# Kernel optimization log

Hardware: AMD Instinct MI355X
Metric: run time of the kernel (lower is better)

The kernel has to match this reference:

```python
import jax, jax.numpy as jnp
import numpy as np

N_NODES = 50000


def _gcn_norm(edge_index, num_nodes):
    # PyG gcn_norm with add_self_loops=True, edge_weight=1
    loops = jnp.arange(num_nodes, dtype=edge_index.dtype)
    src = jnp.concatenate([edge_index[0], loops])
    dst = jnp.concatenate([edge_index[1], loops])
    deg = jax.ops.segment_sum(jnp.ones_like(dst, dtype=jnp.float32), dst,
                              num_segments=num_nodes)
    deg_inv_sqrt = jnp.where(deg > 0, jax.lax.rsqrt(jnp.maximum(deg, 1.0)), 0.0)
    norm = deg_inv_sqrt[src] * deg_inv_sqrt[dst]  # [E + N]
    return src, dst, norm


def _gcn_conv(x, src, dst, norm, W, b, num_nodes):
    h = x @ W                                 # [N, out] dense transform first
    msg = h[src] * norm[:, None]              # gather + scale, [E+N, out]
    out = jax.ops.segment_sum(msg, dst, num_segments=num_nodes)  # scatter-add
    return out + b


def setup_inputs() -> dict:
    key = jax.random.key(0)
    k1, k2, k3, k4, k5 = jax.random.split(key, 5)
    in_ch, out_ch = 128, 64
    hid = 2 * out_ch
    x = jax.random.normal(k1, (N_NODES, in_ch), dtype=jnp.float32)
    edge_index = jax.random.randint(k2, (2, 800000), 0, N_NODES, dtype=jnp.int64)
    # Glorot init like PyG GCNConv
    W1 = jax.random.normal(k3, (in_ch, hid), dtype=jnp.float32) * (1.0 / np.sqrt(in_ch))
    b1 = jnp.zeros((hid,), dtype=jnp.float32)
    W2 = jax.random.normal(k4, (hid, out_ch), dtype=jnp.float32) * (1.0 / np.sqrt(hid))
    b2 = jnp.zeros((out_ch,), dtype=jnp.float32)
    return {"x": x, "edge_index": edge_index, "W1": W1, "b1": b1,
            "W2": W2, "b2": b2}


def reference(x, edge_index, W1, b1, W2, b2):
    num_nodes = x.shape[0]
    src, dst, norm = _gcn_norm(edge_index, num_nodes)
    h = _gcn_conv(x, src, dst, norm, W1, b1, num_nodes)
    h = jax.nn.relu(h)
    return _gcn_conv(h, src, dst, norm, W2, b2, num_nodes)
```

## Files before the change

kernel.cpp:

```cpp
#include <hip/hip_runtime.h>

#define N_NODES 50000
#define N_EDGES 800000
#define IN_CH   128
#define HID     128
#define OUT_CH  64

#define NBUCK 196
#define BUCKW 256
#define XPAD  136

typedef __attribute__((ext_vector_type(8))) short bf16x8;
typedef __attribute__((ext_vector_type(4))) float f32x4;
typedef unsigned short ushort_t;

__device__ __forceinline__ unsigned short f2bf(float f) {
    unsigned u = __float_as_uint(f);
    u += 0x7fffu + ((u >> 16) & 1u);
    return (unsigned short)(u >> 16);
}
__device__ __forceinline__ unsigned pack2(float a, float b) {
    return (unsigned)f2bf(a) | ((unsigned)f2bf(b) << 16);
}
__device__ __forceinline__ float bf_lo(unsigned u) { return __uint_as_float(u << 16); }
__device__ __forceinline__ float bf_hi(unsigned u) { return __uint_as_float(u & 0xffff0000u); }


__global__ void k_zero_small(int* __restrict__ bcnt) {
    if (threadIdx.x < NBUCK) bcnt[threadIdx.x] = 0;
}

__global__ __launch_bounds__(256) void kb_hist(const int* __restrict__ dst,
                                               int* __restrict__ bcnt) {
    __shared__ int lh[NBUCK];
    for (int i = threadIdx.x; i < NBUCK; i += 256) lh[i] = 0;
    __syncthreads();
    int base = blockIdx.x * 8192;
#pragma unroll 4
    for (int k = 0; k < 32; ++k) {
        int e = base + k * 256 + threadIdx.x;
        if (e < N_EDGES) atomicAdd(&lh[dst[e] >> 8], 1);
    }
    __syncthreads();
    for (int i = threadIdx.x; i < NBUCK; i += 256)
        if (lh[i]) atomicAdd(&bcnt[i], lh[i]);
}

__global__ __launch_bounds__(256) void kb_scan(const int* __restrict__ bcnt,
                                               int* __restrict__ bbase,
                                               int* __restrict__ bcur,
                                               int* __restrict__ row_ptr) {
    __shared__ int s[256];
    int t = threadIdx.x;
    int v = (t < NBUCK) ? bcnt[t] : 0;
    s[t] = v;
    __syncthreads();
    for (int off = 1; off < 256; off <<= 1) {
        int u = (t >= off) ? s[t - off] : 0;
        __syncthreads();
        s[t] += u;
        __syncthreads();
    }
    int excl = s[t] - v;
    if (t < NBUCK) { bbase[t] = excl; bcur[t] = excl; }
    if (t == 0) { bbase[NBUCK] = N_EDGES; row_ptr[N_NODES] = N_EDGES; }
}

__global__ __launch_bounds__(256) void kb_scatter(const int* __restrict__ src,
                                                  const int* __restrict__ dst,
                                                  int* __restrict__ bcur,
                                                  uint2* __restrict__ rec) {
    __shared__ int lh[NBUCK];
    __shared__ int gbase[NBUCK];
    for (int i = threadIdx.x; i < NBUCK; i += 256) lh[i] = 0;
    __syncthreads();
    int base = blockIdx.x * 4096;
#pragma unroll 4
    for (int k = 0; k < 16; ++k) {
        int e = base + k * 256 + threadIdx.x;
        if (e < N_EDGES) atomicAdd(&lh[dst[e] >> 8], 1);
    }
    __syncthreads();
    for (int i = threadIdx.x; i < NBUCK; i += 256) {
        int c = lh[i];
        gbase[i] = c ? atomicAdd(&bcur[i], c) : 0;
    }
    __syncthreads();
    for (int i = threadIdx.x; i < NBUCK; i += 256) lh[i] = 0;
    __syncthreads();
#pragma unroll 4
    for (int k = 0; k < 16; ++k) {
        int e = base + k * 256 + threadIdx.x;
        if (e < N_EDGES) {
            int d = dst[e], b = d >> 8;
            int rk = atomicAdd(&lh[b], 1);
            rec[gbase[b] + rk] = make_uint2((unsigned)src[e], (unsigned)d);
        }
    }
}

__global__ __launch_bounds__(256) void kc_csr(const int* __restrict__ bbase,
                                              const uint2* __restrict__ rec,
                                              int* __restrict__ row_ptr,
                                              float* __restrict__ dis,
                                              int* __restrict__ col) {
    __shared__ int lh[BUCKW];
    __shared__ int cur[BUCKW];
    __shared__ int s[BUCKW];
    const int b = blockIdx.x, t = threadIdx.x;
    const int lo = bbase[b], hi = bbase[b + 1];
    lh[t] = 0;
    __syncthreads();
    for (int j = lo + t; j < hi; j += 256)
        atomicAdd(&lh[(int)rec[j].y - (b << 8)], 1);
    __syncthreads();
    int deg = lh[t];
    s[t] = deg;
    __syncthreads();
    for (int off = 1; off < 256; off <<= 1) {
        int u = (t >= off) ? s[t - off] : 0;
        __syncthreads();
        s[t] += u;
        __syncthreads();
    }
    int gp = lo + s[t] - deg;
    int node = (b << 8) + t;
    if (node < N_NODES) {
        row_ptr[node] = gp;
        dis[node] = rsqrtf((float)deg + 1.0f);
    }
    cur[t] = gp;
    __syncthreads();
    for (int j = lo + t; j < hi; j += 256) {
        uint2 r = rec[j];
        int pos = atomicAdd(&cur[(int)r.y - (b << 8)], 1);
        col[pos] = (int)r.x;
    }
}


__global__ __launch_bounds__(256) void k_prep(const float* __restrict__ W1,
                                              const float* __restrict__ W2,
                                              ushort_t* __restrict__ W1t,
                                              ushort_t* __restrict__ W2t) {
    int i = blockIdx.x * 256 + threadIdx.x;
    if (i < 128 * 128) {
        int k = i >> 7, c = i & 127;
        W1t[c * 128 + k] = f2bf(W1[k * 128 + c]);
    } else {
        int j = i - 128 * 128;
        if (j < 128 * 64) {
            int k = j >> 6, c = j & 63;
            W2t[c * 128 + k] = f2bf(W2[k * 64 + c]);
        }
    }
}


__global__ __launch_bounds__(256) void k_gemm1(const float* __restrict__ x,
                                               const ushort_t* __restrict__ W1t,
                                               const float* __restrict__ dis,
                                               ushort_t* __restrict__ g) {
    __shared__ ushort_t xs[64 * XPAD];
    __shared__ ushort_t ws[128 * XPAD];
    const int tid = threadIdx.x;
    const int row0 = blockIdx.x * 64;

    for (int i = tid; i < 64 * 32; i += 256) {
        int r = i >> 5, k4 = (i & 31) << 2;
        int gr = row0 + r;
        float4 v = make_float4(0.f, 0.f, 0.f, 0.f);
        if (gr < N_NODES) v = *(const float4*)&x[(long)gr * IN_CH + k4];
        ushort4 u;
        u.x = f2bf(v.x); u.y = f2bf(v.y); u.z = f2bf(v.z); u.w = f2bf(v.w);
        *(ushort4*)&xs[r * XPAD + k4] = u;
    }
    for (int i = tid; i < 128 * 16; i += 256) {
        int c = i >> 4, seg = i & 15;
        *(uint4*)&ws[c * XPAD + seg * 8] = *(const uint4*)&W1t[c * 128 + seg * 8];
    }
    __syncthreads();

    const int w = tid >> 6, lane = tid & 63;
    const int m = lane & 15, q = lane >> 4;
    const ushort_t* arow = &xs[(w * 16 + m) * XPAD + q * 8];
    const ushort_t* brow = &ws[m * XPAD + q * 8];

    f32x4 acc[8] = {};
#pragma unroll
    for (int k0 = 0; k0 < 128; k0 += 32) {
        bf16x8 a = *(const bf16x8*)(arow + k0);
#pragma unroll
        for (int nt = 0; nt < 8; ++nt) {
            bf16x8 b = *(const bf16x8*)(brow + nt * 16 * XPAD + k0);
            acc[nt] = __builtin_amdgcn_mfma_f32_16x16x32_bf16(a, b, acc[nt], 0, 0, 0);
        }
    }

#pragma unroll
    for (int reg = 0; reg < 4; ++reg) {
        int gr = row0 + w * 16 + q * 4 + reg;
        if (gr < N_NODES) {
            float d = dis[gr];
#pragma unroll
            for (int nt = 0; nt < 8; ++nt)
                g[(long)gr * HID + nt * 16 + m] = f2bf(acc[nt][reg] * d);
        }
    }
}


__global__ __launch_bounds__(256) void k_gemm2(const ushort_t* __restrict__ a1,
                                               const ushort_t* __restrict__ W2t,
                                               const float* __restrict__ dis,
                                               ushort_t* __restrict__ g) {
    __shared__ ushort_t xs[64 * XPAD];
    __shared__ ushort_t ws[64 * XPAD];
    const int tid = threadIdx.x;
    const int row0 = blockIdx.x * 64;

    for (int i = tid; i < 64 * 16; i += 256) {
        int r = i >> 4, seg = i & 15;
        int gr = row0 + r;
        uint4 v = make_uint4(0u, 0u, 0u, 0u);
        if (gr < N_NODES) v = *(const uint4*)&a1[(long)gr * HID + seg * 8];
        *(uint4*)&xs[r * XPAD + seg * 8] = v;
    }
    for (int i = tid; i < 64 * 16; i += 256) {
        int c = i >> 4, seg = i & 15;
        *(uint4*)&ws[c * XPAD + seg * 8] = *(const uint4*)&W2t[c * 128 + seg * 8];
    }
    __syncthreads();

    const int w = tid >> 6, lane = tid & 63;
    const int m = lane & 15, q = lane >> 4;
    const ushort_t* arow = &xs[(w * 16 + m) * XPAD + q * 8];
    const ushort_t* brow = &ws[m * XPAD + q * 8];

    f32x4 acc[4] = {};
#pragma unroll
    for (int k0 = 0; k0 < 128; k0 += 32) {
        bf16x8 a = *(const bf16x8*)(arow + k0);
#pragma unroll
        for (int nt = 0; nt < 4; ++nt) {
            bf16x8 b = *(const bf16x8*)(brow + nt * 16 * XPAD + k0);
            acc[nt] = __builtin_amdgcn_mfma_f32_16x16x32_bf16(a, b, acc[nt], 0, 0, 0);
        }
    }

#pragma unroll
    for (int reg = 0; reg < 4; ++reg) {
        int gr = row0 + w * 16 + q * 4 + reg;
        if (gr < N_NODES) {
            float d = dis[gr];
#pragma unroll
            for (int nt = 0; nt < 4; ++nt)
                g[(long)gr * OUT_CH + nt * 16 + m] = f2bf(acc[nt][reg] * d);
        }
    }
}


__global__ __launch_bounds__(256) void k_agg1(const int* __restrict__ row_ptr,
                                              const int* __restrict__ col,
                                              const float* __restrict__ dis,
                                              const ushort_t* __restrict__ g1,
                                              const float* __restrict__ b1,
                                              ushort_t* __restrict__ a1) {
    int r = blockIdx.x * 4 + (threadIdx.x >> 6);
    if (r >= N_NODES) return;
    const int lane = threadIdx.x & 63;
    const int q = lane >> 4;
    const int seg = lane & 15;
    const int cl = seg << 3;
    const uint4* G = (const uint4*)g1;
    const int beg = row_ptr[r], end = row_ptr[r + 1];

    float acc[8] = {};
    int e = beg + q;
    for (; e + 4 < end; e += 8) {
        int s0 = col[e], s1 = col[e + 4];
        uint4 u0 = G[(long)s0 * 16 + seg];
        uint4 u1 = G[(long)s1 * 16 + seg];
        acc[0] += bf_lo(u0.x); acc[1] += bf_hi(u0.x);
        acc[2] += bf_lo(u0.y); acc[3] += bf_hi(u0.y);
        acc[4] += bf_lo(u0.z); acc[5] += bf_hi(u0.z);
        acc[6] += bf_lo(u0.w); acc[7] += bf_hi(u0.w);
        acc[0] += bf_lo(u1.x); acc[1] += bf_hi(u1.x);
        acc[2] += bf_lo(u1.y); acc[3] += bf_hi(u1.y);
        acc[4] += bf_lo(u1.z); acc[5] += bf_hi(u1.z);
        acc[6] += bf_lo(u1.w); acc[7] += bf_hi(u1.w);
    }
    if (e < end) {
        int s = col[e];
        uint4 u = G[(long)s * 16 + seg];
        acc[0] += bf_lo(u.x); acc[1] += bf_hi(u.x);
        acc[2] += bf_lo(u.y); acc[3] += bf_hi(u.y);
        acc[4] += bf_lo(u.z); acc[5] += bf_hi(u.z);
        acc[6] += bf_lo(u.w); acc[7] += bf_hi(u.w);
    }
#pragma unroll
    for (int off = 16; off < 64; off <<= 1)
#pragma unroll
        for (int j = 0; j < 8; ++j) acc[j] += __shfl_xor(acc[j], off);

    if (q == 0) {
        uint4 u = G[(long)r * 16 + seg];
        acc[0] += bf_lo(u.x); acc[1] += bf_hi(u.x);
        acc[2] += bf_lo(u.y); acc[3] += bf_hi(u.y);
        acc[4] += bf_lo(u.z); acc[5] += bf_hi(u.z);
        acc[6] += bf_lo(u.w); acc[7] += bf_hi(u.w);
        const float d = dis[r];
        float o[8];
#pragma unroll
        for (int j = 0; j < 8; ++j) o[j] = fmaxf(acc[j] * d + b1[cl + j], 0.f);
        uint4 pw;
        pw.x = pack2(o[0], o[1]); pw.y = pack2(o[2], o[3]);
        pw.z = pack2(o[4], o[5]); pw.w = pack2(o[6], o[7]);
        *(uint4*)&a1[(long)r * HID + cl] = pw;
    }
}


__global__ __launch_bounds__(256) void k_agg2(const int* __restrict__ row_ptr,
                                              const int* __restrict__ col,
                                              const float* __restrict__ dis,
                                              const ushort_t* __restrict__ g3,
                                              const float* __restrict__ b2,
                                              float* __restrict__ out) {
    int r = blockIdx.x * 4 + (threadIdx.x >> 6);
    if (r >= N_NODES) return;
    const int lane = threadIdx.x & 63;
    const int q = lane >> 3;
    const int seg = lane & 7;
    const int cl = seg << 3;
    const uint4* G = (const uint4*)g3;
    const int beg = row_ptr[r], end = row_ptr[r + 1];

    float acc[8] = {};
    int e = beg + q;
    for (; e + 8 < end; e += 16) {
        int s0 = col[e], s1 = col[e + 8];
        uint4 u0 = G[(long)s0 * 8 + seg];
        uint4 u1 = G[(long)s1 * 8 + seg];
        acc[0] += bf_lo(u0.x); acc[1] += bf_hi(u0.x);
        acc[2] += bf_lo(u0.y); acc[3] += bf_hi(u0.y);
        acc[4] += bf_lo(u0.z); acc[5] += bf_hi(u0.z);
        acc[6] += bf_lo(u0.w); acc[7] += bf_hi(u0.w);
        acc[0] += bf_lo(u1.x); acc[1] += bf_hi(u1.x);
        acc[2] += bf_lo(u1.y); acc[3] += bf_hi(u1.y);
        acc[4] += bf_lo(u1.z); acc[5] += bf_hi(u1.z);
        acc[6] += bf_lo(u1.w); acc[7] += bf_hi(u1.w);
    }
    if (e < end) {
        int s = col[e];
        uint4 u = G[(long)s * 8 + seg];
        acc[0] += bf_lo(u.x); acc[1] += bf_hi(u.x);
        acc[2] += bf_lo(u.y); acc[3] += bf_hi(u.y);
        acc[4] += bf_lo(u.z); acc[5] += bf_hi(u.z);
        acc[6] += bf_lo(u.w); acc[7] += bf_hi(u.w);
    }
#pragma unroll
    for (int off = 8; off < 64; off <<= 1)
#pragma unroll
        for (int j = 0; j < 8; ++j) acc[j] += __shfl_xor(acc[j], off);

    if (q == 0) {
        uint4 u = G[(long)r * 8 + seg];
        acc[0] += bf_lo(u.x); acc[1] += bf_hi(u.x);
        acc[2] += bf_lo(u.y); acc[3] += bf_hi(u.y);
        acc[4] += bf_lo(u.z); acc[5] += bf_hi(u.z);
        acc[6] += bf_lo(u.w); acc[7] += bf_hi(u.w);
        const float d = dis[r];
        float4 o0, o1;
        o0.x = acc[0] * d + b2[cl + 0];
        o0.y = acc[1] * d + b2[cl + 1];
        o0.z = acc[2] * d + b2[cl + 2];
        o0.w = acc[3] * d + b2[cl + 3];
        o1.x = acc[4] * d + b2[cl + 4];
        o1.y = acc[5] * d + b2[cl + 5];
        o1.z = acc[6] * d + b2[cl + 6];
        o1.w = acc[7] * d + b2[cl + 7];
        *(float4*)&out[(long)r * OUT_CH + cl] = o0;
        *(float4*)&out[(long)r * OUT_CH + cl + 4] = o1;
    }
}


extern "C" void kernel_launch(void* const* d_in, const int* in_sizes, int n_in,
                              void* d_out, int out_size, void* d_ws, size_t ws_size,
                              hipStream_t stream) {
    const float* x   = (const float*)d_in[0];
    const int*   ei  = (const int*)d_in[1];
    const float* W1  = (const float*)d_in[2];
    const float* b1  = (const float*)d_in[3];
    const float* W2  = (const float*)d_in[4];
    const float* b2  = (const float*)d_in[5];
    float* out = (float*)d_out;

    const int* src = ei;
    const int* dst = ei + N_EDGES;

    char* p = (char*)d_ws;
    uint2* rec   = (uint2*)p;             p += (long)N_EDGES * 8;
    int* col     = (int*)p;               p += (long)N_EDGES * 4;
    int* row_ptr = (int*)p;               p += 50064 * 4;
    int* bcnt    = (int*)p;               p += 256 * 4;
    int* bbase   = (int*)p;               p += 256 * 4;
    int* bcur    = (int*)p;               p += 256 * 4;
    float* dis   = (float*)p;             p += 50048 * 4;
    ushort_t* W1t = (ushort_t*)p;         p += 128 * 128 * 2;
    ushort_t* W2t = (ushort_t*)p;         p += 128 * 64 * 2;
    ushort_t* g1  = (ushort_t*)p;         p += (long)N_NODES * HID * 2;
    ushort_t* a1  = (ushort_t*)p;         p += (long)N_NODES * HID * 2;
    ushort_t* g3  = (ushort_t*)p;

    const int B = 256;

    k_zero_small<<<1, B, 0, stream>>>(bcnt);
    k_prep<<<96, B, 0, stream>>>(W1, W2, W1t, W2t);
    kb_hist<<<(N_EDGES + 8191) / 8192, B, 0, stream>>>(dst, bcnt);
    kb_scan<<<1, B, 0, stream>>>(bcnt, bbase, bcur, row_ptr);
    kb_scatter<<<(N_EDGES + 4095) / 4096, B, 0, stream>>>(src, dst, bcur, rec);
    kc_csr<<<NBUCK, B, 0, stream>>>(bbase, rec, row_ptr, dis, col);

    k_gemm1<<<(N_NODES + 63) / 64, B, 0, stream>>>(x, W1t, dis, g1);
    k_agg1<<<(N_NODES + 3) / 4, B, 0, stream>>>(row_ptr, col, dis, g1, b1, a1);
    k_gemm2<<<(N_NODES + 63) / 64, B, 0, stream>>>(a1, W2t, dis, g3);
    k_agg2<<<(N_NODES + 3) / 4, B, 0, stream>>>(row_ptr, col, dis, g3, b2, out);
}
```

Measured before the change: 208.2 us.

## Fuse layer-1 aggregation into second GEMM and fold bucket scan into consumers

Layer-1 aggregation (gather, bias, ReLU) now feeds LDS directly in a new aggregate-then-MFMA kernel, so the a1 intermediate is never written to or read back from global memory. The bucket prefix scan is recomputed inside the scatter and CSR kernels, and the zeroing kernel is merged with weight prep. Together these drop several launches. The edge records are packed into 32 bits (16-bit source plus low 8 bits of destination), halving the record traffic. The trade-off is parallelism: each wave now aggregates 16 rows one after another instead of one row per wave, so the latency of the gathers is hidden less well. The packing also relies on node ids fitting in 16 bits.

```diff
diff --git a/kernel.cpp b/kernel.cpp
--- a/kernel.cpp
+++ b/kernel.cpp
@@ -7,7 +7,6 @@
 #define OUT_CH  64
 
 #define NBUCK 196
-#define BUCKW 256
 #define XPAD  136
 
 typedef __attribute__((ext_vector_type(8))) short bf16x8;
@@ -26,123 +25,15 @@
 __device__ __forceinline__ float bf_hi(unsigned u) { return __uint_as_float(u & 0xffff0000u); }
 
 
-__global__ void k_zero_small(int* __restrict__ bcnt) {
-    if (threadIdx.x < NBUCK) bcnt[threadIdx.x] = 0;
-}
-
-__global__ __launch_bounds__(256) void kb_hist(const int* __restrict__ dst,
-                                               int* __restrict__ bcnt) {
-    __shared__ int lh[NBUCK];
-    for (int i = threadIdx.x; i < NBUCK; i += 256) lh[i] = 0;
-    __syncthreads();
-    int base = blockIdx.x * 8192;
-#pragma unroll 4
-    for (int k = 0; k < 32; ++k) {
-        int e = base + k * 256 + threadIdx.x;
-        if (e < N_EDGES) atomicAdd(&lh[dst[e] >> 8], 1);
-    }
-    __syncthreads();
-    for (int i = threadIdx.x; i < NBUCK; i += 256)
-        if (lh[i]) atomicAdd(&bcnt[i], lh[i]);
-}
-
-__global__ __launch_bounds__(256) void kb_scan(const int* __restrict__ bcnt,
-                                               int* __restrict__ bbase,
-                                               int* __restrict__ bcur,
-                                               int* __restrict__ row_ptr) {
-    __shared__ int s[256];
-    int t = threadIdx.x;
-    int v = (t < NBUCK) ? bcnt[t] : 0;
-    s[t] = v;
-    __syncthreads();
-    for (int off = 1; off < 256; off <<= 1) {
-        int u = (t >= off) ? s[t - off] : 0;
-        __syncthreads();
-        s[t] += u;
-        __syncthreads();
-    }
-    int excl = s[t] - v;
-    if (t < NBUCK) { bbase[t] = excl; bcur[t] = excl; }
-    if (t == 0) { bbase[NBUCK] = N_EDGES; row_ptr[N_NODES] = N_EDGES; }
-}
-
-__global__ __launch_bounds__(256) void kb_scatter(const int* __restrict__ src,
-                                                  const int* __restrict__ dst,
-                                                  int* __restrict__ bcur,
-                                                  uint2* __restrict__ rec) {
-    __shared__ int lh[NBUCK];
-    __shared__ int gbase[NBUCK];
-    for (int i = threadIdx.x; i < NBUCK; i += 256) lh[i] = 0;
-    __syncthreads();
-    int base = blockIdx.x * 4096;
-#pragma unroll 4
-    for (int k = 0; k < 16; ++k) {
-        int e = base + k * 256 + threadIdx.x;
-        if (e < N_EDGES) atomicAdd(&lh[dst[e] >> 8], 1);
-    }
-    __syncthreads();
-    for (int i = threadIdx.x; i < NBUCK; i += 256) {
-        int c = lh[i];
-        gbase[i] = c ? atomicAdd(&bcur[i], c) : 0;
-    }
-    __syncthreads();
-    for (int i = threadIdx.x; i < NBUCK; i += 256) lh[i] = 0;
-    __syncthreads();
-#pragma unroll 4
-    for (int k = 0; k < 16; ++k) {
-        int e = base + k * 256 + threadIdx.x;
-        if (e < N_EDGES) {
-            int d = dst[e], b = d >> 8;
-            int rk = atomicAdd(&lh[b], 1);
-            rec[gbase[b] + rk] = make_uint2((unsigned)src[e], (unsigned)d);
-        }
-    }
-}
-
-__global__ __launch_bounds__(256) void kc_csr(const int* __restrict__ bbase,
-                                              const uint2* __restrict__ rec,
-                                              int* __restrict__ row_ptr,
-                                              float* __restrict__ dis,
-                                              int* __restrict__ col) {
-    __shared__ int lh[BUCKW];
-    __shared__ int cur[BUCKW];
-    __shared__ int s[BUCKW];
-    const int b = blockIdx.x, t = threadIdx.x;
-    const int lo = bbase[b], hi = bbase[b + 1];
-    lh[t] = 0;
-    __syncthreads();
-    for (int j = lo + t; j < hi; j += 256)
-        atomicAdd(&lh[(int)rec[j].y - (b << 8)], 1);
-    __syncthreads();
-    int deg = lh[t];
-    s[t] = deg;
-    __syncthreads();
-    for (int off = 1; off < 256; off <<= 1) {
-        int u = (t >= off) ? s[t - off] : 0;
-        __syncthreads();
-        s[t] += u;
-        __syncthreads();
-    }
-    int gp = lo + s[t] - deg;
-    int node = (b << 8) + t;
-    if (node < N_NODES) {
-        row_ptr[node] = gp;
-        dis[node] = rsqrtf((float)deg + 1.0f);
-    }
-    cur[t] = gp;
-    __syncthreads();
-    for (int j = lo + t; j < hi; j += 256) {
-        uint2 r = rec[j];
-        int pos = atomicAdd(&cur[(int)r.y - (b << 8)], 1);
-        col[pos] = (int)r.x;
-    }
-}
-
-
-__global__ __launch_bounds__(256) void k_prep(const float* __restrict__ W1,
-                                              const float* __restrict__ W2,
-                                              ushort_t* __restrict__ W1t,
-                                              ushort_t* __restrict__ W2t) {
+__global__ __launch_bounds__(256) void k_zero_prep(const float* __restrict__ W1,
+                                                   const float* __restrict__ W2,
+                                                   ushort_t* __restrict__ W1t,
+                                                   ushort_t* __restrict__ W2t,
+                                                   int* __restrict__ bcnt,
+                                                   int* __restrict__ bcur) {
+    if (blockIdx.x == 0) {
+        for (int i = threadIdx.x; i < NBUCK; i += 256) { bcnt[i] = 0; bcur[i] = 0; }
+    }
     int i = blockIdx.x * 256 + threadIdx.x;
     if (i < 128 * 128) {
         int k = i >> 7, c = i & 127;
@@ -157,6 +48,124 @@
 }
 
 
+__global__ __launch_bounds__(256) void kb_hist(const int* __restrict__ dst,
+                                               int* __restrict__ bcnt) {
+    __shared__ int lh[NBUCK];
+    for (int i = threadIdx.x; i < NBUCK; i += 256) lh[i] = 0;
+    __syncthreads();
+    int base = blockIdx.x * 8192;
+#pragma unroll 4
+    for (int k = 0; k < 32; ++k) {
+        int e = base + k * 256 + threadIdx.x;
+        if (e < N_EDGES) atomicAdd(&lh[dst[e] >> 8], 1);
+    }
+    __syncthreads();
+    for (int i = threadIdx.x; i < NBUCK; i += 256)
+        if (lh[i]) atomicAdd(&bcnt[i], lh[i]);
+}
+
+__global__ __launch_bounds__(256) void kb_scatter(const int* __restrict__ src,
+                                                  const int* __restrict__ dst,
+                                                  const int* __restrict__ bcnt,
+                                                  int* __restrict__ bcur,
+                                                  unsigned* __restrict__ rec) {
+    __shared__ int s[256];
+    __shared__ int sbase[NBUCK];
+    __shared__ int lh[NBUCK];
+    __shared__ int gbase[NBUCK];
+    const int t = threadIdx.x;
+    int v = (t < NBUCK) ? bcnt[t] : 0;
+    s[t] = v;
+    __syncthreads();
+    for (int off = 1; off < 256; off <<= 1) {
+        int u = (t >= off) ? s[t - off] : 0;
+        __syncthreads();
+        s[t] += u;
+        __syncthreads();
+    }
+    if (t < NBUCK) sbase[t] = s[t] - v;
+    for (int i = t; i < NBUCK; i += 256) lh[i] = 0;
+    __syncthreads();
+
+    int base = blockIdx.x * 4096;
+#pragma unroll 4
+    for (int k = 0; k < 16; ++k) {
+        int e = base + k * 256 + t;
+        if (e < N_EDGES) atomicAdd(&lh[dst[e] >> 8], 1);
+    }
+    __syncthreads();
+    for (int i = t; i < NBUCK; i += 256) {
+        int c = lh[i];
+        gbase[i] = c ? (sbase[i] + atomicAdd(&bcur[i], c)) : 0;
+    }
+    __syncthreads();
+    for (int i = t; i < NBUCK; i += 256) lh[i] = 0;
+    __syncthreads();
+#pragma unroll 4
+    for (int k = 0; k < 16; ++k) {
+        int e = base + k * 256 + t;
+        if (e < N_EDGES) {
+            int d = dst[e], b = d >> 8;
+            int rk = atomicAdd(&lh[b], 1);
+            rec[gbase[b] + rk] = (unsigned)src[e] | ((unsigned)(d & 255) << 16);
+        }
+    }
+}
+
+__global__ __launch_bounds__(256) void kc_csr(const int* __restrict__ bcnt,
+                                              const unsigned* __restrict__ rec,
+                                              int* __restrict__ row_ptr,
+                                              float* __restrict__ dis,
+                                              int* __restrict__ col) {
+    __shared__ int s[256];
+    __shared__ int lh[256];
+    __shared__ int cur[256];
+    const int b = blockIdx.x, t = threadIdx.x;
+    int v = (t < NBUCK) ? bcnt[t] : 0;
+    s[t] = v;
+    __syncthreads();
+    for (int off = 1; off < 256; off <<= 1) {
+        int u = (t >= off) ? s[t - off] : 0;
+        __syncthreads();
+        s[t] += u;
+        __syncthreads();
+    }
+    __shared__ int lo_s, hi_s;
+    if (t == b) { lo_s = s[t] - v; hi_s = s[t]; }
+    __syncthreads();
+    const int lo = lo_s, hi = hi_s;
+
+    lh[t] = 0;
+    __syncthreads();
+    for (int j = lo + t; j < hi; j += 256)
+        atomicAdd(&lh[rec[j] >> 16], 1);
+    __syncthreads();
+    int deg = lh[t];
+    s[t] = deg;
+    __syncthreads();
+    for (int off = 1; off < 256; off <<= 1) {
+        int u = (t >= off) ? s[t - off] : 0;
+        __syncthreads();
+        s[t] += u;
+        __syncthreads();
+    }
+    int gp = lo + s[t] - deg;
+    int node = (b << 8) + t;
+    if (node < N_NODES) {
+        row_ptr[node] = gp;
+        dis[node] = rsqrtf((float)deg + 1.0f);
+    }
+    if (b == NBUCK - 1 && t == 0) row_ptr[N_NODES] = N_EDGES;
+    cur[t] = gp;
+    __syncthreads();
+    for (int j = lo + t; j < hi; j += 256) {
+        unsigned r = rec[j];
+        int pos = atomicAdd(&cur[r >> 16], 1);
+        col[pos] = (int)(r & 0xffffu);
+    }
+}
+
+
 __global__ __launch_bounds__(256) void k_gemm1(const float* __restrict__ x,
                                                const ushort_t* __restrict__ W1t,
                                                const float* __restrict__ dis,
@@ -210,41 +219,102 @@
 }
 
 
-__global__ __launch_bounds__(256) void k_gemm2(const ushort_t* __restrict__ a1,
+__global__ __launch_bounds__(256) void k_aggmm(const int* __restrict__ row_ptr,
+                                               const int* __restrict__ col,
+                                               const float* __restrict__ dis,
+                                               const ushort_t* __restrict__ g1,
+                                               const float* __restrict__ b1,
                                                const ushort_t* __restrict__ W2t,
-                                               const float* __restrict__ dis,
-                                               ushort_t* __restrict__ g) {
-    __shared__ ushort_t xs[64 * XPAD];
+                                               ushort_t* __restrict__ g3) {
+    __shared__ ushort_t a1s[64 * XPAD];
     __shared__ ushort_t ws[64 * XPAD];
     const int tid = threadIdx.x;
     const int row0 = blockIdx.x * 64;
+    const int w = tid >> 6, lane = tid & 63;
+    const int q = lane >> 4;
+    const int seg = lane & 15;
+    const int cl = seg << 3;
+    const uint4* G = (const uint4*)g1;
 
     for (int i = tid; i < 64 * 16; i += 256) {
-        int r = i >> 4, seg = i & 15;
-        int gr = row0 + r;
-        uint4 v = make_uint4(0u, 0u, 0u, 0u);
-        if (gr < N_NODES) v = *(const uint4*)&a1[(long)gr * HID + seg * 8];
-        *(uint4*)&xs[r * XPAD + seg * 8] = v;
-    }
-    for (int i = tid; i < 64 * 16; i += 256) {
-        int c = i >> 4, seg = i & 15;
-        *(uint4*)&ws[c * XPAD + seg * 8] = *(const uint4*)&W2t[c * 128 + seg * 8];
-    }
-    __syncthreads();
-
-    const int w = tid >> 6, lane = tid & 63;
-    const int m = lane & 15, q = lane >> 4;
-    const ushort_t* arow = &xs[(w * 16 + m) * XPAD + q * 8];
+        int c = i >> 4, sg = i & 15;
+        *(uint4*)&ws[c * XPAD + sg * 8] = *(const uint4*)&W2t[c * 128 + sg * 8];
+    }
+
+    float4 bA = *(const float4*)&b1[cl];
+    float4 bB = *(const float4*)&b1[cl + 4];
+
+    for (int i = 0; i < 16; ++i) {
+        int r = row0 + w * 16 + i;
+        float acc[8] = {};
+        if (r < N_NODES) {
+            const int beg = row_ptr[r], end = row_ptr[r + 1];
+            int e = beg + q;
+            for (; e + 4 < end; e += 8) {
+                int s0 = col[e], s1 = col[e + 4];
+                uint4 u0 = G[(long)s0 * 16 + seg];
+                uint4 u1 = G[(long)s1 * 16 + seg];
+                acc[0] += bf_lo(u0.x); acc[1] += bf_hi(u0.x);
+                acc[2] += bf_lo(u0.y); acc[3] += bf_hi(u0.y);
+                acc[4] += bf_lo(u0.z); acc[5] += bf_hi(u0.z);
+                acc[6] += bf_lo(u0.w); acc[7] += bf_hi(u0.w);
+                acc[0] += bf_lo(u1.x); acc[1] += bf_hi(u1.x);
+                acc[2] += bf_lo(u1.y); acc[3] += bf_hi(u1.y);
+                acc[4] += bf_lo(u1.z); acc[5] += bf_hi(u1.z);
+                acc[6] += bf_lo(u1.w); acc[7] += bf_hi(u1.w);
+            }
+            if (e < end) {
+                int s0 = col[e];
+                uint4 u = G[(long)s0 * 16 + seg];
+                acc[0] += bf_lo(u.x); acc[1] += bf_hi(u.x);
+                acc[2] += bf_lo(u.y); acc[3] += bf_hi(u.y);
+                acc[4] += bf_lo(u.z); acc[5] += bf_hi(u.z);
+                acc[6] += bf_lo(u.w); acc[7] += bf_hi(u.w);
+            }
+        }
+#pragma unroll
+        for (int off = 16; off < 64; off <<= 1)
+#pragma unroll
+            for (int j = 0; j < 8; ++j) acc[j] += __shfl_xor(acc[j], off);
+
+        if (q == 0) {
+            uint4 pw = make_uint4(0u, 0u, 0u, 0u);
+            if (r < N_NODES) {
+                uint4 u = G[(long)r * 16 + seg];
+                acc[0] += bf_lo(u.x); acc[1] += bf_hi(u.x);
+                acc[2] += bf_lo(u.y); acc[3] += bf_hi(u.y);
+                acc[4] += bf_lo(u.z); acc[5] += bf_hi(u.z);
+                acc[6] += bf_lo(u.w); acc[7] += bf_hi(u.w);
+                const float d = dis[r];
+                float o[8];
+                o[0] = fmaxf(acc[0] * d + bA.x, 0.f);
+                o[1] = fmaxf(acc[1] * d + bA.y, 0.f);
+                o[2] = fmaxf(acc[2] * d + bA.z, 0.f);
+                o[3] = fmaxf(acc[3] * d + bA.w, 0.f);
+                o[4] = fmaxf(acc[4] * d + bB.x, 0.f);
+                o[5] = fmaxf(acc[5] * d + bB.y, 0.f);
+                o[6] = fmaxf(acc[6] * d + bB.z, 0.f);
+                o[7] = fmaxf(acc[7] * d + bB.w, 0.f);
+                pw.x = pack2(o[0], o[1]); pw.y = pack2(o[2], o[3]);
+                pw.z = pack2(o[4], o[5]); pw.w = pack2(o[6], o[7]);
+            }
+            *(uint4*)&a1s[(w * 16 + i) * XPAD + cl] = pw;
+        }
+    }
+    __syncthreads();
+
+    const int m = lane & 15;
+    const ushort_t* arow = &a1s[(w * 16 + m) * XPAD + q * 8];
     const ushort_t* brow = &ws[m * XPAD + q * 8];
 
-    f32x4 acc[4] = {};
+    f32x4 acc2[4] = {};
 #pragma unroll
     for (int k0 = 0; k0 < 128; k0 += 32) {
         bf16x8 a = *(const bf16x8*)(arow + k0);
 #pragma unroll
         for (int nt = 0; nt < 4; ++nt) {
             bf16x8 b = *(const bf16x8*)(brow + nt * 16 * XPAD + k0);
-            acc[nt] = __builtin_amdgcn_mfma_f32_16x16x32_bf16(a, b, acc[nt], 0, 0, 0);
+            acc2[nt] = __builtin_amdgcn_mfma_f32_16x16x32_bf16(a, b, acc2[nt], 0, 0, 0);
         }
     }
 
@@ -255,69 +325,8 @@
             float d = dis[gr];
 #pragma unroll
             for (int nt = 0; nt < 4; ++nt)
-                g[(long)gr * OUT_CH + nt * 16 + m] = f2bf(acc[nt][reg] * d);
-        }
-    }
-}
-
-
-__global__ __launch_bounds__(256) void k_agg1(const int* __restrict__ row_ptr,
-                                              const int* __restrict__ col,
-                                              const float* __restrict__ dis,
-                                              const ushort_t* __restrict__ g1,
-                                              const float* __restrict__ b1,
-                                              ushort_t* __restrict__ a1) {
-    int r = blockIdx.x * 4 + (threadIdx.x >> 6);
-    if (r >= N_NODES) return;
-    const int lane = threadIdx.x & 63;
-    const int q = lane >> 4;
-    const int seg = lane & 15;
-    const int cl = seg << 3;
-    const uint4* G = (const uint4*)g1;
-    const int beg = row_ptr[r], end = row_ptr[r + 1];
-
-    float acc[8] = {};
-    int e = beg + q;
-    for (; e + 4 < end; e += 8) {
-        int s0 = col[e], s1 = col[e + 4];
-        uint4 u0 = G[(long)s0 * 16 + seg];
-        uint4 u1 = G[(long)s1 * 16 + seg];
-        acc[0] += bf_lo(u0.x); acc[1] += bf_hi(u0.x);
-        acc[2] += bf_lo(u0.y); acc[3] += bf_hi(u0.y);
-        acc[4] += bf_lo(u0.z); acc[5] += bf_hi(u0.z);
-        acc[6] += bf_lo(u0.w); acc[7] += bf_hi(u0.w);
-        acc[0] += bf_lo(u1.x); acc[1] += bf_hi(u1.x);
-        acc[2] += bf_lo(u1.y); acc[3] += bf_hi(u1.y);
-        acc[4] += bf_lo(u1.z); acc[5] += bf_hi(u1.z);
-        acc[6] += bf_lo(u1.w); acc[7] += bf_hi(u1.w);
-    }
-    if (e < end) {
-        int s = col[e];
-        uint4 u = G[(long)s * 16 + seg];
-        acc[0] += bf_lo(u.x); acc[1] += bf_hi(u.x);
-        acc[2] += bf_lo(u.y); acc[3] += bf_hi(u.y);
-        acc[4] += bf_lo(u.z); acc[5] += bf_hi(u.z);
-        acc[6] += bf_lo(u.w); acc[7] += bf_hi(u.w);
-    }
-#pragma unroll
-    for (int off = 16; off < 64; off <<= 1)
-#pragma unroll
-        for (int j = 0; j < 8; ++j) acc[j] += __shfl_xor(acc[j], off);
-
-    if (q == 0) {
-        uint4 u = G[(long)r * 16 + seg];
-        acc[0] += bf_lo(u.x); acc[1] += bf_hi(u.x);
-        acc[2] += bf_lo(u.y); acc[3] += bf_hi(u.y);
-        acc[4] += bf_lo(u.z); acc[5] += bf_hi(u.z);
-        acc[6] += bf_lo(u.w); acc[7] += bf_hi(u.w);
-        const float d = dis[r];
-        float o[8];
-#pragma unroll
-        for (int j = 0; j < 8; ++j) o[j] = fmaxf(acc[j] * d + b1[cl + j], 0.f);
-        uint4 pw;
-        pw.x = pack2(o[0], o[1]); pw.y = pack2(o[2], o[3]);
-        pw.z = pack2(o[4], o[5]); pw.w = pack2(o[6], o[7]);
-        *(uint4*)&a1[(long)r * HID + cl] = pw;
+                g3[(long)gr * OUT_CH + nt * 16 + m] = f2bf(acc2[nt][reg] * d);
+        }
     }
 }
 
@@ -402,30 +411,25 @@
     const int* dst = ei + N_EDGES;
 
     char* p = (char*)d_ws;
-    uint2* rec   = (uint2*)p;             p += (long)N_EDGES * 8;
+    unsigned* rec = (unsigned*)p;         p += (long)N_EDGES * 4;
     int* col     = (int*)p;               p += (long)N_EDGES * 4;
     int* row_ptr = (int*)p;               p += 50064 * 4;
     int* bcnt    = (int*)p;               p += 256 * 4;
-    int* bbase   = (int*)p;               p += 256 * 4;
     int* bcur    = (int*)p;               p += 256 * 4;
     float* dis   = (float*)p;             p += 50048 * 4;
     ushort_t* W1t = (ushort_t*)p;         p += 128 * 128 * 2;
     ushort_t* W2t = (ushort_t*)p;         p += 128 * 64 * 2;
     ushort_t* g1  = (ushort_t*)p;         p += (long)N_NODES * HID * 2;
-    ushort_t* a1  = (ushort_t*)p;         p += (long)N_NODES * HID * 2;
     ushort_t* g3  = (ushort_t*)p;
 
     const int B = 256;
 
-    k_zero_small<<<1, B, 0, stream>>>(bcnt);
-    k_prep<<<96, B, 0, stream>>>(W1, W2, W1t, W2t);
+    k_zero_prep<<<96, B, 0, stream>>>(W1, W2, W1t, W2t, bcnt, bcur);
     kb_hist<<<(N_EDGES + 8191) / 8192, B, 0, stream>>>(dst, bcnt);
-    kb_scan<<<1, B, 0, stream>>>(bcnt, bbase, bcur, row_ptr);
-    kb_scatter<<<(N_EDGES + 4095) / 4096, B, 0, stream>>>(src, dst, bcur, rec);
-    kc_csr<<<NBUCK, B, 0, stream>>>(bbase, rec, row_ptr, dis, col);
+    kb_scatter<<<(N_EDGES + 4095) / 4096, B, 0, stream>>>(src, dst, bcnt, bcur, rec);
+    kc_csr<<<NBUCK, B, 0, stream>>>(bcnt, rec, row_ptr, dis, col);
 
     k_gemm1<<<(N_NODES + 63) / 64, B, 0, stream>>>(x, W1t, dis, g1);
-    k_agg1<<<(N_NODES + 3) / 4, B, 0, stream>>>(row_ptr, col, dis, g1, b1, a1);
-    k_gemm2<<<(N_NODES + 63) / 64, B, 0, stream>>>(a1, W2t, dis, g3);
+    k_aggmm<<<(N_NODES + 63) / 64, B, 0, stream>>>(row_ptr, col, dis, g1, b1, W2t, g3);
     k_agg2<<<(N_NODES + 3) / 4, B, 0, stream>>>(row_ptr, col, dis, g3, b2, out);
 }
```

After: 218.2 us. 1.05x slower.
